# Optimization experiments

Measured on AMD Instinct MI355X. Metric: run time of the kernel, lower is better.

## Reference

```python
import jax, jax.numpy as jnp
import numpy as np

NEG_FILL = -1000000000.0  # matches torch.full_like(scores, -1e9)


def setup_inputs() -> dict:
    key = jax.random.key(0)
    kq, kk, kv = jax.random.split(key, 3)
    shape = (1, 8, 4096, 64)  # [B, H, L, d]
    Q = jax.random.normal(kq, shape, dtype=jnp.float32)
    K = jax.random.normal(kk, shape, dtype=jnp.float32)
    V = jax.random.normal(kv, shape, dtype=jnp.float32)
    return {"Q": Q, "K": K, "V": V}


def reference(Q, K, V):
    B, H, Lq, d = Q.shape
    Lk = K.shape[-2]
    top_k = max(1, int(Lk * 0.02))  # static: depends only on shape

    # [B,H,Lq,Lk] dense scores
    scores = jnp.einsum('bhqd,bhkd->bhqk', Q, K) / np.sqrt(d).astype(Q.dtype)

    # top-k along last axis
    vals, idx = jax.lax.top_k(scores, top_k)  # [B,H,Lq,k]

    # scatter top-k values into a -1e9-filled matrix (row-wise unique indices)
    N = B * H * Lq
    rows = jnp.arange(N)[:, None]  # [N,1]
    sparse = jnp.full((N, Lk), NEG_FILL, dtype=scores.dtype)
    sparse = sparse.at[rows, idx.reshape(N, top_k)].set(vals.reshape(N, top_k))
    sparse = sparse.reshape(B, H, Lq, Lk)

    attn = jax.nn.softmax(sparse, axis=-1)
    return jnp.einsum('bhqk,bhkd->bhqd', attn, V)
```

## Files before the change

### kernel.cpp

```cpp
#include <hip/hip_runtime.h>
#include <math.h>
#include <stdint.h>

#define LSEQ  4096
#define DIM   64
#define NHEAD 8
#define TOPK  81
#define RSEL  96
#define CAP   128
#define SEGC  64
#define CAP2  336
#define ZGATE 1.59375f
#define ROWS  16
#define NT    512
#define NTC   128
#define TILES (LSEQ/NTC)
#define NBIN2 16

typedef __attribute__((ext_vector_type(8))) short   short8;
typedef __attribute__((ext_vector_type(4))) float   floatx4;
typedef __attribute__((ext_vector_type(2))) double  double2v;

static __device__ __forceinline__ unsigned short f2bf(float f) {
    unsigned int u = __builtin_bit_cast(unsigned int, f);
    u = (u + 0x7fffu + ((u >> 16) & 1u)) >> 16;
    return (unsigned short)u;
}

static __device__ __forceinline__ unsigned int pkbf(float f0, float f1) {
    return __builtin_amdgcn_perm(__builtin_bit_cast(unsigned int, f1),
                                 __builtin_bit_cast(unsigned int, f0),
                                 0x07060302u);
}

__global__ __launch_bounds__(256) void repack_kernel(const float* __restrict__ Kg,
                                                     unsigned short* __restrict__ Kb)
{
    const int w  = threadIdx.x >> 6;
    const int ln = threadIdx.x & 63;
    const int g  = blockIdx.x * 4 + w;
    const int m  = ln & 15, kq = ln >> 4;
    const float* src = Kg + (size_t)g * (16 * DIM) + (size_t)m * DIM + kq * 8;
    float4 f0 = *(const float4*)(src);
    float4 f1 = *(const float4*)(src + 4);
    float4 f2 = *(const float4*)(src + 32);
    float4 f3 = *(const float4*)(src + 36);
    uint4 o0, o1;
    o0.x = pkbf(f0.x, f0.y); o0.y = pkbf(f0.z, f0.w);
    o0.z = pkbf(f1.x, f1.y); o0.w = pkbf(f1.z, f1.w);
    o1.x = pkbf(f2.x, f2.y); o1.y = pkbf(f2.z, f2.w);
    o1.z = pkbf(f3.x, f3.y); o1.w = pkbf(f3.z, f3.w);
    unsigned short* dst = Kb + (size_t)g * 1024;
    *(uint4*)(dst + ln * 8)       = o0;
    *(uint4*)(dst + 512 + ln * 8) = o1;
}

#define K1_SMEM 25152

__global__ __launch_bounds__(NT, 8) void select_kernel(
    const float* __restrict__ Qg, const unsigned short* __restrict__ Kb,
    unsigned int* __restrict__ clg, int* __restrict__ ng)
{
    __shared__ char smem[K1_SMEM] __attribute__((aligned(16)));
    float          (* const Qs)[DIM]        = (float(*)[DIM])            (smem);
    unsigned short (* const preC)[8][SEGC]  = (unsigned short(*)[8][SEGC])(smem + 4096);
    unsigned short (* const clist)[CAP]     = (unsigned short(*)[CAP])   (smem + 20480);
    int            (* const cnt)[8]         = (int(*)[8])                (smem + 24576);
    float*           const gthr             = (float*)                   (smem + 25088);

    const int t  = threadIdx.x;
    const int w  = t >> 6;
    const int ln = t & 63;
    const int m  = ln & 15;
    const int kg = ln >> 4;

    const int h  = blockIdx.x & 7;
    const int r0 = h * LSEQ + (blockIdx.x >> 3) * ROWS;

    if (t < 256) ((float4*)Qs)[t] = ((const float4*)(Qg + (size_t)r0 * DIM))[t];
    __syncthreads();

    #pragma unroll
    for (int rr = 0; rr < 2; ++rr) {
        const int rl = 2 * w + rr;
        float q = Qs[rl][ln];
        float s2 = q * q;
        #pragma unroll
        for (int d2 = 32; d2 >= 1; d2 >>= 1) s2 += __shfl_xor(s2, d2, 64);
        if (ln == 0) gthr[rl] = ZGATE * sqrtf(s2);
    }

    short8 a0, a1;
    #pragma unroll
    for (int j = 0; j < 8; ++j) {
        a0[j] = (short)f2bf(Qs[m][kg * 8 + j]);
        a1[j] = (short)f2bf(Qs[m][32 + kg * 8 + j]);
    }
    __syncthreads();

    const float g0 = gthr[kg * 4 + 0], g1 = gthr[kg * 4 + 1];
    const float g2 = gthr[kg * 4 + 2], g3 = gthr[kg * 4 + 3];
    const float i0 = 25.5f / g0, i1 = 25.5f / g1;
    const float i2 = 25.5f / g2, i3 = 25.5f / g3;

    const unsigned short* __restrict__ Kbh = Kb + (size_t)h * (LSEQ * DIM);

    int c0 = 0, c1 = 0, c2 = 0, c3 = 0;

    auto ldfrag = [&](int tt, short8& b0, short8& b1) {
        const short8* __restrict__ p = (const short8*)(Kbh + (size_t)(tt * 8 + w) * 1024);
        b0 = p[ln];
        b1 = p[64 + ln];
    };
    auto compute_tile = [&](int tt, short8 b0, short8 b1) {
        floatx4 acc = {0.f, 0.f, 0.f, 0.f};
        acc = __builtin_amdgcn_mfma_f32_16x16x32_bf16(a0, b0, acc, 0, 0, 0);
        acc = __builtin_amdgcn_mfma_f32_16x16x32_bf16(a1, b1, acc, 0, 0, 0);
        const int colg = tt * NTC + w * 16 + m;
        const float gr[4] = {g0, g1, g2, g3};
        const float iv[4] = {i0, i1, i2, i3};
        #pragma unroll
        for (int r = 0; r < 4; ++r) {
            int& cr = (r == 0) ? c0 : (r == 1) ? c1 : (r == 2) ? c2 : c3;
            const bool pred = (acc[r] >= gr[r]);
            const unsigned long long mk = __ballot(pred);
            const unsigned int sl = (unsigned int)(mk >> (16 * kg)) & 0xffffu;
            if (pred) {
                int b = (int)fmaf(acc[r], iv[r], -25.5f);
                b = min(NBIN2 - 1, max(0, b));
                const int p = cr + __popc(sl & ((1u << m) - 1u));
                if (p < SEGC) preC[kg * 4 + r][w][p] = (unsigned short)(colg | (b << 12));
            }
            cr += __popc(sl);
        }
    };

    short8 b0a, b1a, b0n, b1n;
    ldfrag(0, b0a, b1a);
    for (int tt = 0; tt < TILES; ++tt) {
        ldfrag(tt + 1 < TILES ? tt + 1 : tt, b0n, b1n);
        compute_tile(tt, b0a, b1a);
        b0a = b0n; b1a = b1n;
    }
    if (m == 0) {
        cnt[kg * 4 + 0][w] = min(c0, SEGC);
        cnt[kg * 4 + 1][w] = min(c1, SEGC);
        cnt[kg * 4 + 2][w] = min(c2, SEGC);
        cnt[kg * 4 + 3][w] = min(c3, SEGC);
    }
    __syncthreads();

    #pragma unroll
    for (int rr = 0; rr < 2; ++rr) {
        const int rl = 2 * w + rr;
        int vv[8], cc[8];
        #pragma unroll
        for (int u = 0; u < 8; ++u) { cc[u] = cnt[rl][u]; vv[u] = preC[rl][u][ln]; }

        int bst = 0;
        #pragma unroll
        for (int s = 8; s >= 1; s >>= 1) {
            const int T = bst + s;
            int cgt = 0;
            #pragma unroll
            for (int u = 0; u < 8; ++u)
                cgt += (int)__popcll(__ballot((ln < cc[u]) && ((vv[u] >> 12) >= T)));
            if (cgt >= RSEL) bst = T;
        }

        int basec = 0;
        #pragma unroll
        for (int u = 0; u < 8; ++u) {
            const bool pv = (ln < cc[u]) && ((vv[u] >> 12) >= bst);
            const unsigned long long mk = __ballot(pv);
            if (pv) {
                const int p = basec + (int)__popcll(mk & ((1ull << ln) - 1ull));
                if (p < CAP) clist[rl][p] = (unsigned short)(vv[u] & 0x0fff);
            }
            basec += (int)__popcll(mk);
        }

        const int grow = r0 + rl;
        if (ln == 0) ng[grow] = min(basec, CAP);
        clg[(size_t)grow * 64 + ln] = ((const unsigned int*)clist[rl])[ln];
    }
}

__global__ __launch_bounds__(NT, 6) void epilogue_kernel(
    const float* __restrict__ Qg, const float* __restrict__ Kg,
    const float* __restrict__ Vg, float* __restrict__ outg,
    const unsigned int* __restrict__ clg, const int* __restrict__ ng)
{
    __shared__ double         sd [8][CAP];
    __shared__ unsigned short cls[8][CAP];

    const int t  = threadIdx.x;
    const int w  = t >> 6;
    const int ln = t & 63;
    const int m  = ln & 15;
    const int kg = ln >> 4;

    const int h    = blockIdx.x & 7;
    const int grow = h * LSEQ + (blockIdx.x >> 3) * 8 + w;
    const float* __restrict__ Kh = Kg + (size_t)h * LSEQ * DIM;
    const float* __restrict__ Vh = Vg + (size_t)h * LSEQ * DIM;
    const float* __restrict__ Qr = Qg + (size_t)grow * DIM;

    const int n = ng[grow];
    ((unsigned int*)cls[w])[ln] = clg[(size_t)grow * 64 + ln];

    sd[w][ln]      = -1e300;
    sd[w][ln + 64] = -1e300;

    const float4 qf = *(const float4*)(Qr + m * 4);
    const double qd0 = qf.x, qd1 = qf.y, qd2 = qf.z, qd3 = qf.w;

    const int nb = min(32, (n + 3) >> 2);
    #pragma unroll 4
    for (int b = 0; b < nb; ++b) {
        const int slot = 4 * b + kg;
        const int c = cls[w][slot] & 0x0fff;
        const float4 kf = *(const float4*)(Kh + (size_t)c * DIM + m * 4);
        double p =      qd0 * (double)kf.x;
        p = fma(qd1, (double)kf.y, p);
        p = fma(qd2, (double)kf.z, p);
        p = fma(qd3, (double)kf.w, p);
        #pragma unroll
        for (int d2 = 8; d2 >= 1; d2 >>= 1) p += __shfl_xor(p, d2, 16);
        if (m == 0 && slot < n) sd[w][slot] = p * 0.125;
    }
    const double s0 = sd[w][ln];
    const double s1 = sd[w][ln + 64];

    double md = fmax(s0, s1);
    #pragma unroll
    for (int d2 = 32; d2 >= 1; d2 >>= 1) md = fmax(md, __shfl_xor(md, d2, 64));

    int r0c = 0, r1c = 0;
    const int nmax = (n + 3) & ~3;
    for (int j = 0; j < nmax; j += 4) {
        double2v A0 = *(const double2v*)&sd[w][j];
        double2v A1 = *(const double2v*)&sd[w][j + 2];
        r0c += (A0[0] > s0) + (A0[1] > s0) + (A1[0] > s0) + (A1[1] > s0);
        r1c += (A0[0] > s1) + (A0[1] > s1) + (A1[0] > s1) + (A1[1] > s1);
    }

    const bool v0 = (ln < n), v1 = (ln + 64 < n);
    float* const wl = (float*)sd[w];
    const float w0 = (v0 && r0c < TOPK) ? expf((float)(s0 - md)) : 0.f;
    const float w1 = (v1 && r1c < TOPK) ? expf((float)(s1 - md)) : 0.f;
    wl[ln]      = w0;
    wl[ln + 64] = w1;
    float zs = w0 + w1;
    #pragma unroll
    for (int d2 = 32; d2 >= 1; d2 >>= 1) zs += __shfl_xor(zs, d2, 64);
    const float zi = 1.f / zs;

    float e0 = 0.f, e1 = 0.f;
    const int npv = (n + 1) & ~1;
    #pragma unroll 2
    for (int i = 0; i < npv; i += 2) {
        float2 wv = *(const float2*)&wl[i];
        unsigned int cp = *(const unsigned int*)&cls[w][i];
        e0 = fmaf(wv.x, Vh[(size_t)(cp & 0xfffu) * DIM + ln], e0);
        e1 = fmaf(wv.y, Vh[(size_t)((cp >> 16) & 0xfffu) * DIM + ln], e1);
    }
    outg[(size_t)grow * DIM + ln] = (e0 + e1) * zi;
}

#define SMEM_BYTES 35456
__global__ __launch_bounds__(NT, 4) void probsparse_mono(
    const float* __restrict__ Qg, const float* __restrict__ Kg,
    const float* __restrict__ Vg, float* __restrict__ outg)
{
    __shared__ char smem[SMEM_BYTES] __attribute__((aligned(16)));
    float          (* const Qs)[DIM]    = (float(*)[DIM])          (smem);
    double         (* const sd)[CAP]    = (double(*)[CAP])         (smem + 4096);
    unsigned short (* const preC)[CAP2] = (unsigned short(*)[CAP2])(smem + 20480);
    unsigned short (* const clist)[CAP] = (unsigned short(*)[CAP]) (smem + 31232);
    int*             const cnt2         = (int*)                   (smem + 35328);
    float*           const gthr         = (float*)(cnt2 + 16);

    const int t = threadIdx.x, w = t >> 6, ln = t & 63, m = ln & 15, kg = ln >> 4;
    const int h  = blockIdx.x & 7;
    const int r0 = h * LSEQ + (blockIdx.x >> 3) * ROWS;
    const float* __restrict__ Kh = Kg + (size_t)h * LSEQ * DIM;
    const float* __restrict__ Vh = Vg + (size_t)h * LSEQ * DIM;

    if (t < 256) ((float4*)Qs)[t] = ((const float4*)(Qg + (size_t)r0 * DIM))[t];
    if (t < ROWS) cnt2[t] = 0;
    __syncthreads();

    #pragma unroll
    for (int rr = 0; rr < 2; ++rr) {
        const int rl = 2 * w + rr;
        float q = Qs[rl][ln];
        float s2 = q * q;
        #pragma unroll
        for (int d2 = 32; d2 >= 1; d2 >>= 1) s2 += __shfl_xor(s2, d2, 64);
        if (ln == 0) gthr[rl] = ZGATE * sqrtf(s2);
    }
    short8 a0, a1;
    #pragma unroll
    for (int j = 0; j < 8; ++j) {
        a0[j] = (short)f2bf(Qs[m][kg * 8 + j]);
        a1[j] = (short)f2bf(Qs[m][32 + kg * 8 + j]);
    }
    __syncthreads();

    const float g0 = gthr[kg * 4 + 0], g1 = gthr[kg * 4 + 1];
    const float g2 = gthr[kg * 4 + 2], g3 = gthr[kg * 4 + 3];
    const float i0 = 25.5f / g0, i1 = 25.5f / g1;
    const float i2 = 25.5f / g2, i3 = 25.5f / g3;

    auto ldfrag = [&](int tt, short8& b0, short8& b1) {
        const float* __restrict__ sf = Kh + (size_t)(tt * NTC + w * 16 + m) * DIM + kg * 8;
        float4 p0 = *(const float4*)(sf);
        float4 p1 = *(const float4*)(sf + 4);
        float4 p2 = *(const float4*)(sf + 32);
        float4 p3 = *(const float4*)(sf + 36);
        uint4 u0, u1;
        u0.x = pkbf(p0.x, p0.y); u0.y = pkbf(p0.z, p0.w);
        u0.z = pkbf(p1.x, p1.y); u0.w = pkbf(p1.z, p1.w);
        u1.x = pkbf(p2.x, p2.y); u1.y = pkbf(p2.z, p2.w);
        u1.z = pkbf(p3.x, p3.y); u1.w = pkbf(p3.z, p3.w);
        b0 = __builtin_bit_cast(short8, u0);
        b1 = __builtin_bit_cast(short8, u1);
    };
    auto compute_tile = [&](int tt, short8 b0, short8 b1) {
        floatx4 acc = {0.f, 0.f, 0.f, 0.f};
        acc = __builtin_amdgcn_mfma_f32_16x16x32_bf16(a0, b0, acc, 0, 0, 0);
        acc = __builtin_amdgcn_mfma_f32_16x16x32_bf16(a1, b1, acc, 0, 0, 0);
        const int colg = tt * NTC + w * 16 + m;
        const float gr[4] = {g0, g1, g2, g3};
        const float iv[4] = {i0, i1, i2, i3};
        #pragma unroll
        for (int r = 0; r < 4; ++r) {
            const bool pred = (acc[r] >= gr[r]);
            unsigned long long mk = __ballot(pred);
            const unsigned int sl = (unsigned int)(mk >> (16 * kg)) & 0xffffu;
            const int tot = __popc(sl);
            const int pre = __popc(sl & ((1u << m) - 1u));
            const int rl  = kg * 4 + r;
            int base = 0;
            if (m == 0 && tot) base = atomicAdd(&cnt2[rl], tot);
            base = __shfl(base, kg * 16, 64);
            if (pred) {
                int b = (int)fmaf(acc[r], iv[r], -25.5f);
                b = min(NBIN2 - 1, max(0, b));
                const int p = base + pre;
                if (p < CAP2) preC[rl][p] = (unsigned short)(colg | (b << 12));
            }
        }
    };

    short8 b0a, b1a, b0n, b1n;
    ldfrag(0, b0a, b1a);
    for (int tt = 0; tt < TILES; ++tt) {
        ldfrag(tt + 1 < TILES ? tt + 1 : tt, b0n, b1n);
        compute_tile(tt, b0a, b1a);
        b0a = b0n; b1a = b1n;
    }
    __syncthreads();

    int n0 = 0, n1 = 0;
    #pragma unroll
    for (int rr = 0; rr < 2; ++rr) {
        const int rl = 2 * w + rr;
        const int n2 = min(cnt2[rl], CAP2);
        int bst = 0;
        #pragma unroll
        for (int s = 8; s >= 1; s >>= 1) {
            const int T = bst + s;
            int cgt = 0;
            #pragma unroll
            for (int u = 0; u < (CAP2 + 63) / 64; ++u) {
                const int i = ln + 64 * u;
                const bool gte = (i < n2) && ((preC[rl][i] >> 12) >= T);
                cgt += (int)__popcll(__ballot(gte));
            }
            if (cgt >= RSEL) bst = T;
        }
        int basec = 0;
        #pragma unroll
        for (int u = 0; u < (CAP2 + 63) / 64; ++u) {
            const int i = ln + 64 * u;
            bool pv = false; unsigned short v = 0;
            if (i < n2) { v = preC[rl][i]; pv = ((v >> 12) >= bst); }
            const unsigned long long mk = __ballot(pv);
            const int pre = __popcll(mk & ((1ull << ln) - 1ull));
            if (pv) {
                const int p = basec + pre;
                if (p < CAP) clist[rl][p] = (unsigned short)(v & 0x0fff);
            }
            basec += (int)__popcll(mk);
        }
        if (rr == 0) n0 = min(basec, CAP); else n1 = min(basec, CAP);
    }

    const int rl0 = 2 * w, rl1 = 2 * w + 1;
    double s00, s01, s10, s11;
    {
        const bool v0 = (ln < n0), v1 = (ln + 64 < n0);
        const int c00 = v0 ? (int)clist[rl0][ln]      : 0;
        const int c01 = v1 ? (int)clist[rl0][ln + 64] : 0;
        const float4* __restrict__ Kp0 = (const float4*)(Kh + (size_t)c00 * DIM);
        const float4* __restrict__ Kp1 = (const float4*)(Kh + (size_t)c01 * DIM);
        double p00 = 0, p01 = 0, p02 = 0, p03 = 0;
        double p10 = 0, p11 = 0, p12 = 0, p13 = 0;
        #pragma unroll
        for (int c4 = 0; c4 < 16; ++c4) {
            float4 q  = *(const float4*)&Qs[rl0][c4 * 4];
            float4 k0 = Kp0[c4];
            float4 k1 = Kp1[c4];
            double& A = (c4 & 3) == 0 ? p00 : (c4 & 3) == 1 ? p01 : (c4 & 3) == 2 ? p02 : p03;
            double& B = (c4 & 3) == 0 ? p10 : (c4 & 3) == 1 ? p11 : (c4 & 3) == 2 ? p12 : p13;
            A = fma((double)q.x, (double)k0.x, A); A = fma((double)q.y, (double)k0.y, A);
            A = fma((double)q.z, (double)k0.z, A); A = fma((double)q.w, (double)k0.w, A);
            B = fma((double)q.x, (double)k1.x, B); B = fma((double)q.y, (double)k1.y, B);
            B = fma((double)q.z, (double)k1.z, B); B = fma((double)q.w, (double)k1.w, B);
        }
        s00 = v0 ? ((p00 + p01) + (p02 + p03)) * 0.125 : -1e300;
        s01 = v1 ? ((p10 + p11) + (p12 + p13)) * 0.125 : -1e300;
        sd[rl0][ln]      = s00;
        sd[rl0][ln + 64] = s01;
    }
    {
        const bool v0 = (ln < n1), v1 = (ln + 64 < n1);
        const int c10 = v0 ? (int)clist[rl1][ln]      : 0;
        const int c11 = v1 ? (int)clist[rl1][ln + 64] : 0;
        const float4* __restrict__ Kp0 = (const float4*)(Kh + (size_t)c10 * DIM);
        const float4* __restrict__ Kp1 = (const float4*)(Kh + (size_t)c11 * DIM);
        double p00 = 0, p01 = 0, p02 = 0, p03 = 0;
        double p10 = 0, p11 = 0, p12 = 0, p13 = 0;
        #pragma unroll
        for (int c4 = 0; c4 < 16; ++c4) {
            float4 q  = *(const float4*)&Qs[rl1][c4 * 4];
            float4 k0 = Kp0[c4];
            float4 k1 = Kp1[c4];
            double& A = (c4 & 3) == 0 ? p00 : (c4 & 3) == 1 ? p01 : (c4 & 3) == 2 ? p02 : p03;
            double& B = (c4 & 3) == 0 ? p10 : (c4 & 3) == 1 ? p11 : (c4 & 3) == 2 ? p12 : p13;
            A = fma((double)q.x, (double)k0.x, A); A = fma((double)q.y, (double)k0.y, A);
            A = fma((double)q.z, (double)k0.z, A); A = fma((double)q.w, (double)k0.w, A);
            B = fma((double)q.x, (double)k1.x, B); B = fma((double)q.y, (double)k1.y, B);
            B = fma((double)q.z, (double)k1.z, B); B = fma((double)q.w, (double)k1.w, B);
        }
        s10 = v0 ? ((p00 + p01) + (p02 + p03)) * 0.125 : -1e300;
        s11 = v1 ? ((p10 + p11) + (p12 + p13)) * 0.125 : -1e300;
        sd[rl1][ln]      = s10;
        sd[rl1][ln + 64] = s11;
    }
    double md0 = fmax(s00, s01), md1 = fmax(s10, s11);
    #pragma unroll
    for (int d2 = 32; d2 >= 1; d2 >>= 1) {
        md0 = fmax(md0, __shfl_xor(md0, d2, 64));
        md1 = fmax(md1, __shfl_xor(md1, d2, 64));
    }
    int r00 = 0, r01 = 0, r10 = 0, r11 = 0;
    const int nmax = (max(n0, n1) + 3) & ~3;
    for (int j = 0; j < nmax; j += 4) {
        double2v A0 = *(const double2v*)&sd[rl0][j];
        double2v A1 = *(const double2v*)&sd[rl0][j + 2];
        double2v B0 = *(const double2v*)&sd[rl1][j];
        double2v B1 = *(const double2v*)&sd[rl1][j + 2];
        r00 += (A0[0] > s00) + (A0[1] > s00) + (A1[0] > s00) + (A1[1] > s00);
        r01 += (A0[0] > s01) + (A0[1] > s01) + (A1[0] > s01) + (A1[1] > s01);
        r10 += (B0[0] > s10) + (B0[1] > s10) + (B1[0] > s10) + (B1[1] > s10);
        r11 += (B0[0] > s11) + (B0[1] > s11) + (B1[0] > s11) + (B1[1] > s11);
    }
    float* const wl0 = (float*)sd[rl0];
    float* const wl1 = (float*)sd[rl1];
    float w00 = (ln      < n0 && r00 < TOPK) ? expf((float)(s00 - md0)) : 0.f;
    float w01 = (ln + 64 < n0 && r01 < TOPK) ? expf((float)(s01 - md0)) : 0.f;
    float w10 = (ln      < n1 && r10 < TOPK) ? expf((float)(s10 - md1)) : 0.f;
    float w11 = (ln + 64 < n1 && r11 < TOPK) ? expf((float)(s11 - md1)) : 0.f;
    wl0[ln]      = w00;  wl0[ln + 64] = w01;
    wl1[ln]      = w10;  wl1[ln + 64] = w11;
    float zs0 = w00 + w01, zs1 = w10 + w11;
    #pragma unroll
    for (int d2 = 32; d2 >= 1; d2 >>= 1) {
        zs0 += __shfl_xor(zs0, d2, 64);
        zs1 += __shfl_xor(zs1, d2, 64);
    }
    const float zi0 = 1.f / zs0, zi1 = 1.f / zs1;
    float e00 = 0.f, e01 = 0.f, e10 = 0.f, e11 = 0.f;
    const int npv = (max(n0, n1) + 1) & ~1;
    #pragma unroll 2
    for (int i = 0; i < npv; i += 2) {
        float2 wv0 = *(const float2*)&wl0[i];
        float2 wv1 = *(const float2*)&wl1[i];
        unsigned int cp0 = *(const unsigned int*)&clist[rl0][i];
        unsigned int cp1 = *(const unsigned int*)&clist[rl1][i];
        e00 = fmaf(wv0.x, Vh[(size_t)(cp0 & 0xfffu) * DIM + ln], e00);
        e01 = fmaf(wv0.y, Vh[(size_t)((cp0 >> 16) & 0xfffu) * DIM + ln], e01);
        e10 = fmaf(wv1.x, Vh[(size_t)(cp1 & 0xfffu) * DIM + ln], e10);
        e11 = fmaf(wv1.y, Vh[(size_t)((cp1 >> 16) & 0xfffu) * DIM + ln], e11);
    }
    outg[(size_t)(r0 + rl0) * DIM + ln] = (e00 + e01) * zi0;
    outg[(size_t)(r0 + rl1) * DIM + ln] = (e10 + e11) * zi1;
}

extern "C" void kernel_launch(void* const* d_in, const int* in_sizes, int n_in,
                              void* d_out, int out_size, void* d_ws, size_t ws_size,
                              hipStream_t stream) {
    const float* Q = (const float*)d_in[0];
    const float* K = (const float*)d_in[1];
    const float* V = (const float*)d_in[2];
    float* out = (float*)d_out;
    (void)in_sizes; (void)n_in; (void)out_size;

    const size_t off_cl = (size_t)4 << 20;
    const size_t off_n  = off_cl + ((size_t)8 << 20);
    const size_t need   = off_n + (size_t)NHEAD * LSEQ * 4;

    if (d_ws != nullptr && ws_size >= need) {
        unsigned short* Kb  = (unsigned short*)d_ws;
        unsigned int*   clg = (unsigned int*)((char*)d_ws + off_cl);
        int*            ng  = (int*)((char*)d_ws + off_n);
        hipLaunchKernelGGL(repack_kernel,   dim3(512),  dim3(256), 0, stream, K, Kb);
        hipLaunchKernelGGL(select_kernel,   dim3(2048), dim3(NT),  0, stream, Q, Kb, clg, ng);
        hipLaunchKernelGGL(epilogue_kernel, dim3(4096), dim3(NT),  0, stream, Q, K, V, out, clg, ng);
    } else {
        hipLaunchKernelGGL(probsparse_mono, dim3(2048), dim3(NT),  0, stream, Q, K, V, out);
    }
}
```

Baseline: 265.8 us.

## Fuse candidate selection and exact rescoring epilogue into one kernel

Merges the select and epilogue kernels, so the candidate lists and counts stay in shared memory and no longer round-trip through global workspace. Each wave now rescores, ranks and accumulates V for two rows, reusing the preC shared-memory region for the double-precision scores. This removes one kernel launch and the clg/ng global traffic. In exchange, the epilogue phase runs at the select kernel's occupancy with two interleaved rows per wave, and loop bounds use the maximum of the two rows' candidate counts.

```diff
diff --git a/kernel.cpp b/kernel.cpp
--- a/kernel.cpp
+++ b/kernel.cpp
@@ -57,13 +57,15 @@
 
 #define K1_SMEM 25152
 
-__global__ __launch_bounds__(NT, 8) void select_kernel(
+__global__ __launch_bounds__(NT, 8) void fused_kernel(
     const float* __restrict__ Qg, const unsigned short* __restrict__ Kb,
-    unsigned int* __restrict__ clg, int* __restrict__ ng)
+    const float* __restrict__ Kg, const float* __restrict__ Vg,
+    float* __restrict__ outg)
 {
     __shared__ char smem[K1_SMEM] __attribute__((aligned(16)));
     float          (* const Qs)[DIM]        = (float(*)[DIM])            (smem);
     unsigned short (* const preC)[8][SEGC]  = (unsigned short(*)[8][SEGC])(smem + 4096);
+    double         (* const sd)[CAP]        = (double(*)[CAP])           (smem + 4096);
     unsigned short (* const clist)[CAP]     = (unsigned short(*)[CAP])   (smem + 20480);
     int            (* const cnt)[8]         = (int(*)[8])                (smem + 24576);
     float*           const gthr             = (float*)                   (smem + 25088);
@@ -76,6 +78,8 @@
 
     const int h  = blockIdx.x & 7;
     const int r0 = h * LSEQ + (blockIdx.x >> 3) * ROWS;
+    const float* __restrict__ Kh = Kg + (size_t)h * LSEQ * DIM;
+    const float* __restrict__ Vh = Vg + (size_t)h * LSEQ * DIM;
 
     if (t < 256) ((float4*)Qs)[t] = ((const float4*)(Qg + (size_t)r0 * DIM))[t];
     __syncthreads();
@@ -150,6 +154,7 @@
     }
     __syncthreads();
 
+    int n0 = 0, n1 = 0;
     #pragma unroll
     for (int rr = 0; rr < 2; ++rr) {
         const int rl = 2 * w + rr;
@@ -179,93 +184,88 @@
             }
             basec += (int)__popcll(mk);
         }
-
-        const int grow = r0 + rl;
-        if (ln == 0) ng[grow] = min(basec, CAP);
-        clg[(size_t)grow * 64 + ln] = ((const unsigned int*)clist[rl])[ln];
-    }
-}
-
-__global__ __launch_bounds__(NT, 6) void epilogue_kernel(
-    const float* __restrict__ Qg, const float* __restrict__ Kg,
-    const float* __restrict__ Vg, float* __restrict__ outg,
-    const unsigned int* __restrict__ clg, const int* __restrict__ ng)
-{
-    __shared__ double         sd [8][CAP];
-    __shared__ unsigned short cls[8][CAP];
-
-    const int t  = threadIdx.x;
-    const int w  = t >> 6;
-    const int ln = t & 63;
-    const int m  = ln & 15;
-    const int kg = ln >> 4;
-
-    const int h    = blockIdx.x & 7;
-    const int grow = h * LSEQ + (blockIdx.x >> 3) * 8 + w;
-    const float* __restrict__ Kh = Kg + (size_t)h * LSEQ * DIM;
-    const float* __restrict__ Vh = Vg + (size_t)h * LSEQ * DIM;
-    const float* __restrict__ Qr = Qg + (size_t)grow * DIM;
-
-    const int n = ng[grow];
-    ((unsigned int*)cls[w])[ln] = clg[(size_t)grow * 64 + ln];
-
-    sd[w][ln]      = -1e300;
-    sd[w][ln + 64] = -1e300;
-
-    const float4 qf = *(const float4*)(Qr + m * 4);
-    const double qd0 = qf.x, qd1 = qf.y, qd2 = qf.z, qd3 = qf.w;
-
-    const int nb = min(32, (n + 3) >> 2);
-    #pragma unroll 4
-    for (int b = 0; b < nb; ++b) {
-        const int slot = 4 * b + kg;
-        const int c = cls[w][slot] & 0x0fff;
-        const float4 kf = *(const float4*)(Kh + (size_t)c * DIM + m * 4);
-        double p =      qd0 * (double)kf.x;
-        p = fma(qd1, (double)kf.y, p);
-        p = fma(qd2, (double)kf.z, p);
-        p = fma(qd3, (double)kf.w, p);
-        #pragma unroll
-        for (int d2 = 8; d2 >= 1; d2 >>= 1) p += __shfl_xor(p, d2, 16);
-        if (m == 0 && slot < n) sd[w][slot] = p * 0.125;
-    }
-    const double s0 = sd[w][ln];
-    const double s1 = sd[w][ln + 64];
-
-    double md = fmax(s0, s1);
-    #pragma unroll
-    for (int d2 = 32; d2 >= 1; d2 >>= 1) md = fmax(md, __shfl_xor(md, d2, 64));
-
-    int r0c = 0, r1c = 0;
-    const int nmax = (n + 3) & ~3;
+        if (rr == 0) n0 = min(basec, CAP); else n1 = min(basec, CAP);
+    }
+
+    const int rl0 = 2 * w, rl1 = 2 * w + 1;
+
+    #pragma unroll
+    for (int rr = 0; rr < 2; ++rr) {
+        const int rl = 2 * w + rr;
+        const int n  = rr ? n1 : n0;
+        sd[rl][ln]      = -1e300;
+        sd[rl][ln + 64] = -1e300;
+        const float4 qf = *(const float4*)&Qs[rl][m * 4];
+        const double qd0 = qf.x, qd1 = qf.y, qd2 = qf.z, qd3 = qf.w;
+        const int nb = min(32, (n + 3) >> 2);
+        #pragma unroll 4
+        for (int b = 0; b < nb; ++b) {
+            const int slot = 4 * b + kg;
+            const int c = clist[rl][slot] & 0x0fff;
+            const float4 kf = *(const float4*)(Kh + (size_t)c * DIM + m * 4);
+            double p =      qd0 * (double)kf.x;
+            p = fma(qd1, (double)kf.y, p);
+            p = fma(qd2, (double)kf.z, p);
+            p = fma(qd3, (double)kf.w, p);
+            #pragma unroll
+            for (int d2 = 8; d2 >= 1; d2 >>= 1) p += __shfl_xor(p, d2, 16);
+            if (m == 0 && slot < n) sd[rl][slot] = p * 0.125;
+        }
+    }
+    const double s00 = sd[rl0][ln], s01 = sd[rl0][ln + 64];
+    const double s10 = sd[rl1][ln], s11 = sd[rl1][ln + 64];
+
+    double md0 = fmax(s00, s01), md1 = fmax(s10, s11);
+    #pragma unroll
+    for (int d2 = 32; d2 >= 1; d2 >>= 1) {
+        md0 = fmax(md0, __shfl_xor(md0, d2, 64));
+        md1 = fmax(md1, __shfl_xor(md1, d2, 64));
+    }
+
+    int r00 = 0, r01 = 0, r10 = 0, r11 = 0;
+    const int nmax = (max(n0, n1) + 3) & ~3;
     for (int j = 0; j < nmax; j += 4) {
-        double2v A0 = *(const double2v*)&sd[w][j];
-        double2v A1 = *(const double2v*)&sd[w][j + 2];
-        r0c += (A0[0] > s0) + (A0[1] > s0) + (A1[0] > s0) + (A1[1] > s0);
-        r1c += (A0[0] > s1) + (A0[1] > s1) + (A1[0] > s1) + (A1[1] > s1);
-    }
-
-    const bool v0 = (ln < n), v1 = (ln + 64 < n);
-    float* const wl = (float*)sd[w];
-    const float w0 = (v0 && r0c < TOPK) ? expf((float)(s0 - md)) : 0.f;
-    const float w1 = (v1 && r1c < TOPK) ? expf((float)(s1 - md)) : 0.f;
-    wl[ln]      = w0;
-    wl[ln + 64] = w1;
-    float zs = w0 + w1;
-    #pragma unroll
-    for (int d2 = 32; d2 >= 1; d2 >>= 1) zs += __shfl_xor(zs, d2, 64);
-    const float zi = 1.f / zs;
-
-    float e0 = 0.f, e1 = 0.f;
-    const int npv = (n + 1) & ~1;
+        double2v A0 = *(const double2v*)&sd[rl0][j];
+        double2v A1 = *(const double2v*)&sd[rl0][j + 2];
+        double2v B0 = *(const double2v*)&sd[rl1][j];
+        double2v B1 = *(const double2v*)&sd[rl1][j + 2];
+        r00 += (A0[0] > s00) + (A0[1] > s00) + (A1[0] > s00) + (A1[1] > s00);
+        r01 += (A0[0] > s01) + (A0[1] > s01) + (A1[0] > s01) + (A1[1] > s01);
+        r10 += (B0[0] > s10) + (B0[1] > s10) + (B1[0] > s10) + (B1[1] > s10);
+        r11 += (B0[0] > s11) + (B0[1] > s11) + (B1[0] > s11) + (B1[1] > s11);
+    }
+
+    float* const wl0 = (float*)sd[rl0];
+    float* const wl1 = (float*)sd[rl1];
+    float w00 = (ln      < n0 && r00 < TOPK) ? expf((float)(s00 - md0)) : 0.f;
+    float w01 = (ln + 64 < n0 && r01 < TOPK) ? expf((float)(s01 - md0)) : 0.f;
+    float w10 = (ln      < n1 && r10 < TOPK) ? expf((float)(s10 - md1)) : 0.f;
+    float w11 = (ln + 64 < n1 && r11 < TOPK) ? expf((float)(s11 - md1)) : 0.f;
+    wl0[ln]      = w00;  wl0[ln + 64] = w01;
+    wl1[ln]      = w10;  wl1[ln + 64] = w11;
+    float zs0 = w00 + w01, zs1 = w10 + w11;
+    #pragma unroll
+    for (int d2 = 32; d2 >= 1; d2 >>= 1) {
+        zs0 += __shfl_xor(zs0, d2, 64);
+        zs1 += __shfl_xor(zs1, d2, 64);
+    }
+    const float zi0 = 1.f / zs0, zi1 = 1.f / zs1;
+
+    float e00 = 0.f, e01 = 0.f, e10 = 0.f, e11 = 0.f;
+    const int npv = (max(n0, n1) + 1) & ~1;
     #pragma unroll 2
     for (int i = 0; i < npv; i += 2) {
-        float2 wv = *(const float2*)&wl[i];
-        unsigned int cp = *(const unsigned int*)&cls[w][i];
-        e0 = fmaf(wv.x, Vh[(size_t)(cp & 0xfffu) * DIM + ln], e0);
-        e1 = fmaf(wv.y, Vh[(size_t)((cp >> 16) & 0xfffu) * DIM + ln], e1);
-    }
-    outg[(size_t)grow * DIM + ln] = (e0 + e1) * zi;
+        float2 wv0 = *(const float2*)&wl0[i];
+        float2 wv1 = *(const float2*)&wl1[i];
+        unsigned int cp0 = *(const unsigned int*)&clist[rl0][i];
+        unsigned int cp1 = *(const unsigned int*)&clist[rl1][i];
+        e00 = fmaf(wv0.x, Vh[(size_t)(cp0 & 0xfffu) * DIM + ln], e00);
+        e01 = fmaf(wv0.y, Vh[(size_t)((cp0 >> 16) & 0xfffu) * DIM + ln], e01);
+        e10 = fmaf(wv1.x, Vh[(size_t)(cp1 & 0xfffu) * DIM + ln], e10);
+        e11 = fmaf(wv1.y, Vh[(size_t)((cp1 >> 16) & 0xfffu) * DIM + ln], e11);
+    }
+    outg[(size_t)(r0 + rl0) * DIM + ln] = (e00 + e01) * zi0;
+    outg[(size_t)(r0 + rl1) * DIM + ln] = (e10 + e11) * zi1;
 }
 
 #define SMEM_BYTES 35456
@@ -509,18 +509,13 @@
     float* out = (float*)d_out;
     (void)in_sizes; (void)n_in; (void)out_size;
 
-    const size_t off_cl = (size_t)4 << 20;
-    const size_t off_n  = off_cl + ((size_t)8 << 20);
-    const size_t need   = off_n + (size_t)NHEAD * LSEQ * 4;
+    const size_t need = (size_t)NHEAD * LSEQ * DIM * sizeof(unsigned short);
 
     if (d_ws != nullptr && ws_size >= need) {
-        unsigned short* Kb  = (unsigned short*)d_ws;
-        unsigned int*   clg = (unsigned int*)((char*)d_ws + off_cl);
-        int*            ng  = (int*)((char*)d_ws + off_n);
-        hipLaunchKernelGGL(repack_kernel,   dim3(512),  dim3(256), 0, stream, K, Kb);
-        hipLaunchKernelGGL(select_kernel,   dim3(2048), dim3(NT),  0, stream, Q, Kb, clg, ng);
-        hipLaunchKernelGGL(epilogue_kernel, dim3(4096), dim3(NT),  0, stream, Q, K, V, out, clg, ng);
+        unsigned short* Kb = (unsigned short*)d_ws;
+        hipLaunchKernelGGL(repack_kernel, dim3(512),  dim3(256), 0, stream, K, Kb);
+        hipLaunchKernelGGL(fused_kernel,  dim3(2048), dim3(NT),  0, stream, Q, Kb, K, V, out);
     } else {
-        hipLaunchKernelGGL(probsparse_mono, dim3(2048), dim3(NT),  0, stream, Q, K, V, out);
+        hipLaunchKernelGGL(probsparse_mono, dim3(2048), dim3(NT), 0, stream, Q, K, V, out);
     }
 }
```

Result: faster. 254.0 us (-4.4%).
